# Kernel tuning notes

Measured on AMD Instinct MI355X. Metric: run time of the kernel, lower is better.

The kernel has to match this reference:

```python
import jax, jax.numpy as jnp
import numpy as np

B, L, D = 4, 4096, 1024
K = D // 4

def setup_inputs() -> dict:
    key = jax.random.key(0)
    ks = jax.random.split(key, 16)
    def w(k, sh):
        return jax.random.normal(k, sh, dtype=jnp.float32) * 0.02
    return {
        'x': jax.random.normal(ks[0], (B, L, D), dtype=jnp.float32),
        'Wk1': w(ks[1], (D, D)), 'bk1': jnp.zeros((D,), jnp.float32),
        'Wk2': w(ks[2], (D, K * 4)), 'bk2': jnp.zeros((K * 4,), jnp.float32),
        'Wq1': w(ks[3], (D, D)), 'bq1': jnp.zeros((D,), jnp.float32),
        'Wq2': w(ks[4], (D, K * 4)), 'bq2': jnp.zeros((K * 4,), jnp.float32),
        'Wv': w(ks[5], (D, D)), 'bv': jnp.zeros((D,), jnp.float32),
        'gamma': jnp.ones((D,), jnp.float32), 'beta': jnp.zeros((D,), jnp.float32),
        'Wo': w(ks[6], (D, D)), 'bo': jnp.zeros((D,), jnp.float32),
    }

def _normalize(q, eps=1e-12):
    n = jnp.sqrt(jnp.sum(q * q, axis=-1, keepdims=True))
    return q / jnp.maximum(n, eps)

def _quat_conj(q):
    return q * jnp.asarray([1., -1., -1., -1.], dtype=q.dtype)

def _quat_mul(q1, q2):
    w1, x1, y1, z1 = q1[..., 0], q1[..., 1], q1[..., 2], q1[..., 3]
    w2, x2, y2, z2 = q2[..., 0], q2[..., 1], q2[..., 2], q2[..., 3]
    w = w1 * w2 - x1 * x2 - y1 * y2 - z1 * z2
    x = w1 * x2 + x1 * w2 + y1 * z2 - z1 * y2
    y = w1 * y2 - x1 * z2 + y1 * w2 + z1 * x2
    z = w1 * z2 + x1 * y2 - y1 * x2 + z1 * w2
    return jnp.stack([w, x, y, z], axis=-1)

def _quat_rotate(q, v):
    return _quat_mul(_quat_mul(q, v), _quat_conj(q))

def _mlp(x, W1, b1, W2, b2):
    h = jax.nn.gelu(x @ W1 + b1, approximate=False)
    return h @ W2 + b2

def _layernorm(x, g, b, eps=1e-5):
    mu = jnp.mean(x, axis=-1, keepdims=True)
    var = jnp.var(x, axis=-1, keepdims=True)
    return (x - mu) * jax.lax.rsqrt(var + eps) * g + b

def reference(x, Wk1, bk1, Wk2, bk2, Wq1, bq1, Wq2, bq2, Wv, bv, gamma, beta, Wo, bo):
    b, l, d = x.shape
    k = d // 4
    key_q = _normalize(_mlp(x, Wk1, bk1, Wk2, bk2).reshape(b, l, k, 4))
    query_q = _normalize(_mlp(x, Wq1, bq1, Wq2, bq2).reshape(b, l, k, 4))
    value = (x @ Wv + bv).reshape(b, l, k, 4)
    rotated = _quat_rotate(key_q, value)            # [B,L,K,4]
    memory = jnp.cumsum(rotated, axis=1)            # prefix-sum memory
    retrieved = _quat_rotate(_quat_conj(query_q), memory).reshape(b, l, d)
    norm = jnp.sqrt(jnp.arange(1, l + 1, dtype=x.dtype)).reshape(1, l, 1)
    out = _layernorm(retrieved / norm, gamma, beta) @ Wo + bo
    return x + out
```

## Files before the change

kernel.cpp:

```cpp
#include <hip/hip_runtime.h>
#include <cstddef>
#include <cstdint>

static constexpr int Bb  = 4;
static constexpr int Ll  = 4096;
static constexpr int Mm  = 16384;
static constexpr int KK  = 1024;
static constexpr int NT2 = 16;

typedef __attribute__((ext_vector_type(8))) short short8;
typedef __attribute__((ext_vector_type(4))) float f32x4;

#define AS1C(p) ((const __attribute__((address_space(1))) void*)(p))
#define AS3(p)  ((__attribute__((address_space(3))) void*)(p))

__device__ __forceinline__ float b2f(unsigned short u) {
    union { unsigned int i; float f; } c; c.i = ((unsigned int)u) << 16; return c.f;
}
__device__ __forceinline__ unsigned short f2b(float f) {
    union { float f; unsigned int i; } c; c.f = f;
    unsigned int r = c.i + 0x7fffu + ((c.i >> 16) & 1u);
    return (unsigned short)(r >> 16);
}
__device__ __forceinline__ float4 qmul(const float4 a, const float4 b) {
    float4 r;
    r.x = a.x * b.x - a.y * b.y - a.z * b.z - a.w * b.w;
    r.y = a.x * b.y + a.y * b.x + a.z * b.w - a.w * b.z;
    r.z = a.x * b.z - a.y * b.w + a.z * b.x + a.w * b.y;
    r.w = a.x * b.w + a.y * b.z - a.z * b.y + a.w * b.x;
    return r;
}
__device__ __forceinline__ float4 qconj(const float4 a) {
    return make_float4(a.x, -a.y, -a.z, -a.w);
}
__device__ __forceinline__ float4 qnorm(const float4 a) {
    float n = sqrtf(a.x * a.x + a.y * a.y + a.z * a.z + a.w * a.w);
    float inv = 1.0f / fmaxf(n, 1e-12f);
    return make_float4(a.x * inv, a.y * inv, a.z * inv, a.w * inv);
}
__device__ __forceinline__ float gelu_fast(float v) {
    const float a = fabsf(v) * 0.70710678118654752f;
    const float t = 1.0f / (1.0f + 0.3275911f * a);
    const float p = t * (0.254829592f + t * (-0.284496736f + t * (1.421413741f
                   + t * (-1.453152027f + t * 1.061405429f))));
    const float e = __expf(-a * a);
    const float erfa = 1.0f - p * e;
    return 0.5f * v * (1.0f + copysignf(erfa, v));
}

__global__ __launch_bounds__(256)
void conv_k(const float* __restrict__ src, unsigned short* __restrict__ dst, int n4)
{
    const int i = blockIdx.x * 256 + threadIdx.x;
    if (i >= n4) return;
    const float4 v = reinterpret_cast<const float4*>(src)[i];
    ushort4 o;
    o.x = f2b(v.x); o.y = f2b(v.y); o.z = f2b(v.z); o.w = f2b(v.w);
    reinterpret_cast<ushort4*>(dst)[i] = o;
}

__global__ __launch_bounds__(256)
void wtrans_k(const float* __restrict__ src, unsigned short* __restrict__ dst)
{
    __shared__ float t[32][33];
    const int tx = threadIdx.x, ty = threadIdx.y;
    const int n0 = blockIdx.x * 32, k0 = blockIdx.y * 32;
    #pragma unroll
    for (int j = ty; j < 32; j += 8)
        t[j][tx] = src[(size_t)(k0 + j) * 1024 + n0 + tx];
    __syncthreads();
    #pragma unroll
    for (int j = ty; j < 32; j += 8)
        dst[(size_t)(n0 + j) * 1024 + k0 + tx] = f2b(t[tx][j]);
}

__global__ __launch_bounds__(256)
void bcat_k(const float* __restrict__ bk1, const float* __restrict__ bq1,
            const float* __restrict__ bv,  const float* __restrict__ bk2,
            const float* __restrict__ bq2, float* __restrict__ b1,
            float* __restrict__ b2)
{
    const int i = blockIdx.x * 256 + threadIdx.x;
    if (i < 3072) b1[i] = (i < 1024) ? bk1[i] : (i < 2048 ? bq1[i - 1024] : bv[i - 2048]);
    if (i < 2048) b2[i] = (i < 1024) ? bk2[i] : bq2[i - 1024];
}

template<int MODE>
__global__ __launch_bounds__(512, 2)
void gemm256_k(const unsigned short* __restrict__ A, int astride,
               const unsigned short* __restrict__ BT,
               const float* __restrict__ bias,
               const float* __restrict__ resid,
               unsigned short* __restrict__ outH,
               float* __restrict__ outF,
               int Nn)
{
    extern __shared__ char smem[];
    const int tid  = threadIdx.x;
    const int lane = tid & 63;
    const int w    = tid >> 6;
    const int wr   = w >> 2;
    const int wc   = w & 3;

    const int nwg = gridDim.x;
    const int cpx = nwg >> 3;
    const int bid = blockIdx.x;
    const int swz = (bid & 7) * cpx + (bid >> 3);
    const int nTN = Nn >> 8;
    const int m0  = (swz / nTN) << 8;
    const int n0  = (swz % nTN) << 8;
    const int aoff = (MODE == 1 && n0 >= 1024) ? 1024 : 0;

    const unsigned short* pA[2];
    const unsigned short* pB[2];
    #pragma unroll
    for (int c2 = 0; c2 < 2; ++c2) {
        const int s = c2 * 512 + tid;
        const int line = s >> 3;
        const int v = (s & 7) ^ (line & 7);
        const int r = 2 * line + (v >> 2);
        const int kcs = v & 3;
        pA[c2] = A + (size_t)(m0 + r) * astride + aoff + kcs * 8;
        pB[c2] = BT + (size_t)(n0 + r) * KK + kcs * 8;
    }

    auto STAGE_UNIT = [&](int cdst, int matB, int khs, int t1) {
        const int ks = t1 * 64 + khs * 32;
        #pragma unroll
        for (int c2 = 0; c2 < 2; ++c2) {
            __builtin_amdgcn_global_load_lds(
                AS1C((matB ? pB[c2] : pA[c2]) + ks),
                AS3(smem + cdst * 65536 + matB * 32768 + khs * 16384 + c2 * 8192 + w * 1024),
                16, 0, 0);
        }
    };

    const int kc = lane >> 4;
    const int rl = lane & 15;
    int offA[8], offB[4];
    #pragma unroll
    for (int mi = 0; mi < 8; ++mi) {
        const int r = wr * 128 + mi * 16 + rl;
        offA[mi] = (r >> 1) * 128 + (((((r & 1) << 2) | kc) ^ ((r >> 1) & 7)) << 4);
    }
    #pragma unroll
    for (int ni = 0; ni < 4; ++ni) {
        const int r = wc * 64 + ni * 16 + rl;
        offB[ni] = 32768 + (r >> 1) * 128 + (((((r & 1) << 2) | kc) ^ ((r >> 1) & 7)) << 4);
    }

    f32x4 acc[8][4] = {};
    short8 af[8];

    auto PHASE = [&](int c, int kh, int nh, int su, int t1, int vm) {
        const int base = c * 65536 + kh * 16384;
        if (nh == 0) {
            #pragma unroll
            for (int mi = 0; mi < 8; ++mi)
                af[mi] = *(const short8*)(smem + base + offA[mi]);
        }
        const short8 b0 = *(const short8*)(smem + base + offB[2 * nh + 0]);
        const short8 b1 = *(const short8*)(smem + base + offB[2 * nh + 1]);
        if (su >= 0) STAGE_UNIT(c ^ 1, su & 1, su >> 1, t1);
        __builtin_amdgcn_s_setprio(1);
        #pragma unroll
        for (int mi = 0; mi < 8; ++mi) {
            acc[mi][2 * nh + 0] = __builtin_amdgcn_mfma_f32_16x16x32_bf16(af[mi], b0, acc[mi][2 * nh + 0], 0, 0, 0);
            acc[mi][2 * nh + 1] = __builtin_amdgcn_mfma_f32_16x16x32_bf16(af[mi], b1, acc[mi][2 * nh + 1], 0, 0, 0);
        }
        __builtin_amdgcn_s_setprio(0);
        if (vm == 4)      asm volatile("s_waitcnt vmcnt(4)" ::: "memory");
        else if (vm == 0) asm volatile("s_waitcnt vmcnt(0)" ::: "memory");
        if (vm >= -1) __builtin_amdgcn_s_barrier();
    };

    STAGE_UNIT(0, 0, 0, 0);
    STAGE_UNIT(0, 1, 0, 0);
    STAGE_UNIT(0, 0, 1, 0);
    STAGE_UNIT(0, 1, 1, 0);
    asm volatile("s_waitcnt vmcnt(0)" ::: "memory");
    __builtin_amdgcn_s_barrier();

    for (int t = 0; t < NT2 - 1; ++t) {
        const int c = t & 1;
        PHASE(c, 0, 0, 0, t + 1, 4);
        PHASE(c, 0, 1, 1, t + 1, 4);
        PHASE(c, 1, 0, 2, t + 1, 4);
        PHASE(c, 1, 1, 3, t + 1, 4);
    }
    PHASE(1, 0, 0, -1, 0, -1);
    PHASE(1, 0, 1, -1, 0, 0);
    PHASE(1, 1, 0, -1, 0, -2);
    PHASE(1, 1, 1, -1, 0, -2);
    __syncthreads();

    const int colb = n0 + wc * 64 + rl;
    const int rowb = m0 + wr * 128 + kc * 4;
    float bv[4];
    #pragma unroll
    for (int ni = 0; ni < 4; ++ni) bv[ni] = bias[colb + ni * 16];

    const bool bf16out = (MODE == 1) || (MODE == 0 && n0 < 2048);
    if (bf16out) {
        unsigned short* eb = (unsigned short*)smem;
        const int er = tid >> 2, eq = tid & 3;
        #pragma unroll
        for (int pass = 0; pass < 2; ++pass) {
            if (wr == pass) {
                #pragma unroll
                for (int ni = 0; ni < 4; ++ni) {
                    const int col = wc * 64 + ni * 16 + rl;
                    #pragma unroll
                    for (int mi = 0; mi < 8; ++mi)
                        #pragma unroll
                        for (int rr = 0; rr < 4; ++rr) {
                            float v = acc[mi][ni][rr] + bv[ni];
                            if (MODE == 0) v = gelu_fast(v);
                            eb[(mi * 16 + kc * 4 + rr) * 264 + col] = f2b(v);
                        }
                }
            }
            __syncthreads();
            const size_t grow = (size_t)(m0 + pass * 128 + er) * 2048 + n0 + eq * 64;
            #pragma unroll
            for (int j = 0; j < 8; ++j) {
                *(uint4*)(outH + grow + j * 8) =
                    *(const uint4*)(eb + er * 264 + eq * 64 + j * 8);
            }
            __syncthreads();
        }
    } else {
        #pragma unroll
        for (int ni = 0; ni < 4; ++ni) {
            const int col = colb + ni * 16;
            #pragma unroll
            for (int mi = 0; mi < 8; ++mi) {
                #pragma unroll
                for (int rr = 0; rr < 4; ++rr) {
                    float v = acc[mi][ni][rr] + bv[ni];
                    const int row = rowb + mi * 16 + rr;
                    if (MODE == 0) {
                        outF[(size_t)row * 1024 + (col - 2048)] = v;
                    } else {
                        const size_t ix = (size_t)row * 1024 + col;
                        outF[ix] = v + resid[ix];
                    }
                }
            }
        }
    }
}

__global__ __launch_bounds__(256)
void rotfuse_k(const unsigned short* __restrict__ qb2, float* __restrict__ val,
               float* __restrict__ part)
{
    const int idx = blockIdx.x * 256 + threadIdx.x;
    const int kq  = idx & 255;
    const int ch  = (idx >> 8) & 63;
    const int b   = idx >> 14;
    const int row0 = b * Ll + ch * 64;
    float4 s = make_float4(0.f, 0.f, 0.f, 0.f);
    for (int i = 0; i < 64; ++i) {
        const int row = row0 + i;
        const ushort4 qu = *reinterpret_cast<const ushort4*>(qb2 + (size_t)row * 2048 + kq * 4);
        const float4 q = qnorm(make_float4(b2f(qu.x), b2f(qu.y), b2f(qu.z), b2f(qu.w)));
        float4* vp = reinterpret_cast<float4*>(val + (size_t)row * 1024 + kq * 4);
        const float4 r = qmul(qmul(q, *vp), qconj(q));
        *vp = r;
        s.x += r.x; s.y += r.y; s.z += r.z; s.w += r.w;
    }
    *reinterpret_cast<float4*>(part + (size_t)idx * 4) = s;
}

__global__ __launch_bounds__(256)
void scan2_k(float* __restrict__ part)
{
    const int idx = blockIdx.x * 256 + threadIdx.x;
    const int kq = idx & 255, b = idx >> 8;
    float4 run = make_float4(0.f, 0.f, 0.f, 0.f);
    for (int c = 0; c < 64; ++c) {
        float4* p = reinterpret_cast<float4*>(part + (((size_t)(b * 64 + c)) * 256 + kq) * 4);
        const float4 t = *p;
        *p = run;
        run.x += t.x; run.y += t.y; run.z += t.z; run.w += t.w;
    }
}

__global__ __launch_bounds__(256)
void scan3_k(float* __restrict__ val, const float* __restrict__ part)
{
    const int idx = blockIdx.x * 256 + threadIdx.x;
    const int kq  = idx & 255;
    const int ch  = (idx >> 8) & 63;
    const int b   = idx >> 14;
    const int row0 = b * Ll + ch * 64;
    float4 run = *reinterpret_cast<const float4*>(part + (size_t)idx * 4);
    for (int i = 0; i < 64; ++i) {
        float4* vp = reinterpret_cast<float4*>(val + (size_t)(row0 + i) * 1024 + kq * 4);
        const float4 v = *vp;
        run.x += v.x; run.y += v.y; run.z += v.z; run.w += v.w;
        *vp = run;
    }
}

__global__ __launch_bounds__(256)
void retrieve_ln_k(const float* __restrict__ mem, const unsigned short* __restrict__ qb2,
                   const float* __restrict__ gamma, const float* __restrict__ beta,
                   unsigned short* __restrict__ out)
{
    const int row = blockIdx.x;
    const int l   = row & (Ll - 1);
    const int t   = threadIdx.x;
    const size_t base = (size_t)row * 1024 + t * 4;

    const ushort4 qu = *reinterpret_cast<const ushort4*>(qb2 + (size_t)row * 2048 + 1024 + t * 4);
    const float4 q = qnorm(make_float4(b2f(qu.x), b2f(qu.y), b2f(qu.z), b2f(qu.w)));
    const float4 m4 = *reinterpret_cast<const float4*>(mem + base);
    float4 r = qmul(qmul(qconj(q), m4), q);

    const float inv = 1.0f / sqrtf((float)(l + 1));
    r.x *= inv; r.y *= inv; r.z *= inv; r.w *= inv;

    float s  = r.x + r.y + r.z + r.w;
    float ss = r.x * r.x + r.y * r.y + r.z * r.z + r.w * r.w;
    #pragma unroll
    for (int off = 32; off > 0; off >>= 1) {
        s  += __shfl_xor(s, off);
        ss += __shfl_xor(ss, off);
    }
    __shared__ float red[2][4];
    const int wid = t >> 6, lane = t & 63;
    if (lane == 0) { red[0][wid] = s; red[1][wid] = ss; }
    __syncthreads();
    const float sum = red[0][0] + red[0][1] + red[0][2] + red[0][3];
    const float ssq = red[1][0] + red[1][1] + red[1][2] + red[1][3];
    const float mu  = sum * (1.0f / 1024.0f);
    const float var = ssq * (1.0f / 1024.0f) - mu * mu;
    const float sc  = rsqrtf(var + 1e-5f);

    const float4 g4 = *reinterpret_cast<const float4*>(gamma + t * 4);
    const float4 b4 = *reinterpret_cast<const float4*>(beta  + t * 4);
    ushort4 o;
    o.x = f2b((r.x - mu) * sc * g4.x + b4.x);
    o.y = f2b((r.y - mu) * sc * g4.y + b4.y);
    o.z = f2b((r.z - mu) * sc * g4.z + b4.z);
    o.w = f2b((r.w - mu) * sc * g4.w + b4.w);
    *reinterpret_cast<ushort4*>(out + base) = o;
}

extern "C" void kernel_launch(void* const* d_in, const int* in_sizes, int n_in,
                              void* d_out, int out_size, void* d_ws, size_t ws_size,
                              hipStream_t stream)
{
    const float* x     = (const float*)d_in[0];
    const float* Wk1   = (const float*)d_in[1];
    const float* bk1   = (const float*)d_in[2];
    const float* Wk2   = (const float*)d_in[3];
    const float* bk2   = (const float*)d_in[4];
    const float* Wq1   = (const float*)d_in[5];
    const float* bq1   = (const float*)d_in[6];
    const float* Wq2   = (const float*)d_in[7];
    const float* bq2   = (const float*)d_in[8];
    const float* Wv    = (const float*)d_in[9];
    const float* bv    = (const float*)d_in[10];
    const float* gamma = (const float*)d_in[11];
    const float* beta  = (const float*)d_in[12];
    const float* Wo    = (const float*)d_in[13];
    const float* bo    = (const float*)d_in[14];
    float* out = (float*)d_out;

    const size_t TD = (size_t)Mm * 1024;
    const size_t DD = (size_t)1024 * 1024;

    unsigned short* qb2   = (unsigned short*)d_ws;
    unsigned short* xb    = qb2;
    unsigned short* wcat1 = qb2 + TD;
    unsigned short* h     = qb2 + 2 * TD;
    float*          bufB  = (float*)(h + 2 * TD);
    unsigned short* wcat2 = (unsigned short*)(bufB + TD);
    unsigned short* woT   = wcat2 + 2 * DD;
    float*          bcat1 = (float*)(woT + DD);
    float*          bcat2 = bcat1 + 3072;
    float*          part  = bcat2 + 2048;

    const dim3 blk(256);
    const dim3 tblk(32, 8);
    const dim3 tgrid(32, 32);

    (void)hipFuncSetAttribute((const void*)gemm256_k<0>, hipFuncAttributeMaxDynamicSharedMemorySize, 131072);
    (void)hipFuncSetAttribute((const void*)gemm256_k<1>, hipFuncAttributeMaxDynamicSharedMemorySize, 131072);
    (void)hipFuncSetAttribute((const void*)gemm256_k<2>, hipFuncAttributeMaxDynamicSharedMemorySize, 131072);

    conv_k<<<(int)(TD / 4 / 256), blk, 0, stream>>>(x, xb, (int)(TD / 4));
    wtrans_k<<<tgrid, tblk, 0, stream>>>(Wk1, wcat1);
    wtrans_k<<<tgrid, tblk, 0, stream>>>(Wq1, wcat1 + DD);
    wtrans_k<<<tgrid, tblk, 0, stream>>>(Wv,  wcat1 + 2 * DD);
    wtrans_k<<<tgrid, tblk, 0, stream>>>(Wk2, wcat2);
    wtrans_k<<<tgrid, tblk, 0, stream>>>(Wq2, wcat2 + DD);
    wtrans_k<<<tgrid, tblk, 0, stream>>>(Wo,  woT);
    bcat_k<<<12, blk, 0, stream>>>(bk1, bq1, bv, bk2, bq2, bcat1, bcat2);

    gemm256_k<0><<<64 * 12, 512, 131072, stream>>>(xb, 1024, wcat1, bcat1, nullptr, h, bufB, 3072);
    gemm256_k<1><<<64 * 8, 512, 131072, stream>>>(h, 2048, wcat2, bcat2, nullptr, qb2, nullptr, 2048);

    rotfuse_k<<<256, blk, 0, stream>>>(qb2, bufB, part);
    scan2_k<<<4, blk, 0, stream>>>(part);
    scan3_k<<<256, blk, 0, stream>>>(bufB, part);

    retrieve_ln_k<<<Mm, blk, 0, stream>>>(bufB, qb2, gamma, beta, h);

    gemm256_k<2><<<64 * 4, 512, 131072, stream>>>(h, 1024, woT, bo, x, nullptr, out, 1024);
}
```

Before: 480.6 us.

## Restructure GEMM pipeline, store value in bf16, fuse scan with retrieve-layernorm

```diff
diff --git a/kernel.cpp b/kernel.cpp
--- a/kernel.cpp
+++ b/kernel.cpp
@@ -6,7 +6,8 @@
 static constexpr int Ll  = 4096;
 static constexpr int Mm  = 16384;
 static constexpr int KK  = 1024;
-static constexpr int NT2 = 16;
+static constexpr int NCH = 128;
+static constexpr int CHL = 32;
 
 typedef __attribute__((ext_vector_type(8))) short short8;
 typedef __attribute__((ext_vector_type(4))) float f32x4;
@@ -21,6 +22,12 @@
     union { float f; unsigned int i; } c; c.f = f;
     unsigned int r = c.i + 0x7fffu + ((c.i >> 16) & 1u);
     return (unsigned short)(r >> 16);
+}
+__device__ __forceinline__ float4 bq2f(ushort4 u) {
+    return make_float4(b2f(u.x), b2f(u.y), b2f(u.z), b2f(u.w));
+}
+__device__ __forceinline__ ushort4 f2bq(float4 v) {
+    ushort4 o; o.x = f2b(v.x); o.y = f2b(v.y); o.z = f2b(v.z); o.w = f2b(v.w); return o;
 }
 __device__ __forceinline__ float4 qmul(const float4 a, const float4 b) {
     float4 r;
@@ -54,9 +61,7 @@
     const int i = blockIdx.x * 256 + threadIdx.x;
     if (i >= n4) return;
     const float4 v = reinterpret_cast<const float4*>(src)[i];
-    ushort4 o;
-    o.x = f2b(v.x); o.y = f2b(v.y); o.z = f2b(v.z); o.w = f2b(v.w);
-    reinterpret_cast<ushort4*>(dst)[i] = o;
+    reinterpret_cast<ushort4*>(dst)[i] = f2bq(v);
 }
 
 __global__ __launch_bounds__(256)
@@ -92,6 +97,7 @@
                const float* __restrict__ bias,
                const float* __restrict__ resid,
                unsigned short* __restrict__ outH,
+               unsigned short* __restrict__ outV,
                float* __restrict__ outF,
                int Nn)
 {
@@ -124,13 +130,12 @@
         pB[c2] = BT + (size_t)(n0 + r) * KK + kcs * 8;
     }
 
-    auto STAGE_UNIT = [&](int cdst, int matB, int khs, int t1) {
-        const int ks = t1 * 64 + khs * 32;
+    auto STAGE = [&](int matB, int slot, int kh, int koff) {
         #pragma unroll
         for (int c2 = 0; c2 < 2; ++c2) {
             __builtin_amdgcn_global_load_lds(
-                AS1C((matB ? pB[c2] : pA[c2]) + ks),
-                AS3(smem + cdst * 65536 + matB * 32768 + khs * 16384 + c2 * 8192 + w * 1024),
+                AS1C((matB ? pB[c2] : pA[c2]) + koff),
+                AS3(smem + matB * 65536 + slot * 32768 + kh * 16384 + c2 * 8192 + w * 1024),
                 16, 0, 0);
         }
     };
@@ -146,62 +151,89 @@
     #pragma unroll
     for (int ni = 0; ni < 4; ++ni) {
         const int r = wc * 64 + ni * 16 + rl;
-        offB[ni] = 32768 + (r >> 1) * 128 + (((((r & 1) << 2) | kc) ^ ((r >> 1) & 7)) << 4);
+        offB[ni] = (r >> 1) * 128 + (((((r & 1) << 2) | kc) ^ ((r >> 1) & 7)) << 4);
     }
 
     f32x4 acc[8][4] = {};
     short8 af[8];
 
-    auto PHASE = [&](int c, int kh, int nh, int su, int t1, int vm) {
-        const int base = c * 65536 + kh * 16384;
-        if (nh == 0) {
+    auto PHASE = [&](int slot, int kh, int nih, int smat, int sslot, int skh,
+                     int skoff, int vm) {
+        const int ub = slot * 32768 + kh * 16384;
+        if (nih == 0) {
             #pragma unroll
             for (int mi = 0; mi < 8; ++mi)
-                af[mi] = *(const short8*)(smem + base + offA[mi]);
-        }
-        const short8 b0 = *(const short8*)(smem + base + offB[2 * nh + 0]);
-        const short8 b1 = *(const short8*)(smem + base + offB[2 * nh + 1]);
-        if (su >= 0) STAGE_UNIT(c ^ 1, su & 1, su >> 1, t1);
+                af[mi] = *(const short8*)(smem + ub + offA[mi]);
+        }
+        const short8 b0 = *(const short8*)(smem + 65536 + ub + offB[2 * nih + 0]);
+        const short8 b1 = *(const short8*)(smem + 65536 + ub + offB[2 * nih + 1]);
+        if (smat >= 0) STAGE(smat, sslot, skh, skoff);
+        __builtin_amdgcn_s_barrier();
         __builtin_amdgcn_s_setprio(1);
         #pragma unroll
         for (int mi = 0; mi < 8; ++mi) {
-            acc[mi][2 * nh + 0] = __builtin_amdgcn_mfma_f32_16x16x32_bf16(af[mi], b0, acc[mi][2 * nh + 0], 0, 0, 0);
-            acc[mi][2 * nh + 1] = __builtin_amdgcn_mfma_f32_16x16x32_bf16(af[mi], b1, acc[mi][2 * nh + 1], 0, 0, 0);
+            acc[mi][2 * nih + 0] = __builtin_amdgcn_mfma_f32_16x16x32_bf16(af[mi], b0, acc[mi][2 * nih + 0], 0, 0, 0);
+            acc[mi][2 * nih + 1] = __builtin_amdgcn_mfma_f32_16x16x32_bf16(af[mi], b1, acc[mi][2 * nih + 1], 0, 0, 0);
         }
         __builtin_amdgcn_s_setprio(0);
         if (vm == 4)      asm volatile("s_waitcnt vmcnt(4)" ::: "memory");
         else if (vm == 0) asm volatile("s_waitcnt vmcnt(0)" ::: "memory");
-        if (vm >= -1) __builtin_amdgcn_s_barrier();
+        __builtin_amdgcn_s_barrier();
     };
 
-    STAGE_UNIT(0, 0, 0, 0);
-    STAGE_UNIT(0, 1, 0, 0);
-    STAGE_UNIT(0, 0, 1, 0);
-    STAGE_UNIT(0, 1, 1, 0);
-    asm volatile("s_waitcnt vmcnt(0)" ::: "memory");
+    STAGE(0, 0, 0, 0);  STAGE(1, 0, 0, 0);
+    STAGE(0, 0, 1, 32); STAGE(1, 0, 1, 32);
+    STAGE(0, 1, 0, 64); STAGE(1, 1, 0, 64);
+    asm volatile("s_waitcnt vmcnt(4)" ::: "memory");
     __builtin_amdgcn_s_barrier();
 
-    for (int t = 0; t < NT2 - 1; ++t) {
-        const int c = t & 1;
-        PHASE(c, 0, 0, 0, t + 1, 4);
-        PHASE(c, 0, 1, 1, t + 1, 4);
-        PHASE(c, 1, 0, 2, t + 1, 4);
-        PHASE(c, 1, 1, 3, t + 1, 4);
-    }
-    PHASE(1, 0, 0, -1, 0, -1);
-    PHASE(1, 0, 1, -1, 0, 0);
-    PHASE(1, 1, 0, -1, 0, -2);
-    PHASE(1, 1, 1, -1, 0, -2);
+    for (int i = 0; i < 7; ++i) {
+        const int kb = i * 128;
+        PHASE(0, 0, 0,  0, 1, 1, kb + 96,  -1);
+        PHASE(0, 0, 1,  1, 1, 1, kb + 96,  -1);
+        PHASE(0, 1, 0,  0, 0, 0, kb + 128, -1);
+        PHASE(0, 1, 1,  1, 0, 0, kb + 128,  4);
+        PHASE(1, 0, 0,  0, 0, 1, kb + 160, -1);
+        PHASE(1, 0, 1,  1, 0, 1, kb + 160, -1);
+        PHASE(1, 1, 0,  0, 1, 0, kb + 192, -1);
+        PHASE(1, 1, 1,  1, 1, 0, kb + 192,  4);
+    }
+    PHASE(0, 0, 0,  0, 1, 1, 992, -1);
+    PHASE(0, 0, 1,  1, 1, 1, 992, -1);
+    PHASE(0, 1, 0, -1, 0, 0, 0,   -1);
+    PHASE(0, 1, 1, -1, 0, 0, 0,    0);
+    PHASE(1, 0, 0, -1, 0, 0, 0,   -1);
+    PHASE(1, 0, 1, -1, 0, 0, 0,   -1);
+    PHASE(1, 1, 0, -1, 0, 0, 0,   -1);
+    PHASE(1, 1, 1, -1, 0, 0, 0,   -1);
     __syncthreads();
 
     const int colb = n0 + wc * 64 + rl;
-    const int rowb = m0 + wr * 128 + kc * 4;
     float bv[4];
     #pragma unroll
     for (int ni = 0; ni < 4; ++ni) bv[ni] = bias[colb + ni * 16];
 
-    const bool bf16out = (MODE == 1) || (MODE == 0 && n0 < 2048);
-    if (bf16out) {
+    if (MODE == 2) {
+        const int rowb = m0 + wr * 128 + kc * 4;
+        #pragma unroll
+        for (int ni = 0; ni < 4; ++ni) {
+            const int col = colb + ni * 16;
+            #pragma unroll
+            for (int mi = 0; mi < 8; ++mi) {
+                #pragma unroll
+                for (int rr = 0; rr < 4; ++rr) {
+                    const int row = rowb + mi * 16 + rr;
+                    const size_t ix = (size_t)row * 1024 + col;
+                    outF[ix] = acc[mi][ni][rr] + bv[ni] + resid[ix];
+                }
+            }
+        }
+    } else {
+        const bool dogelu = (MODE == 0) && (n0 < 2048);
+        unsigned short* dst;
+        int stride, col0;
+        if (MODE == 0 && n0 >= 2048) { dst = outV; stride = 1024; col0 = n0 - 2048; }
+        else                         { dst = outH; stride = 2048; col0 = n0; }
         unsigned short* eb = (unsigned short*)smem;
         const int er = tid >> 2, eq = tid & 3;
         #pragma unroll
@@ -211,63 +243,42 @@
                 for (int ni = 0; ni < 4; ++ni) {
                     const int col = wc * 64 + ni * 16 + rl;
                     #pragma unroll
-                    for (int mi = 0; mi < 8; ++mi)
+                    for (int mi = 0; mi < 8; ++mi) {
                         #pragma unroll
                         for (int rr = 0; rr < 4; ++rr) {
                             float v = acc[mi][ni][rr] + bv[ni];
-                            if (MODE == 0) v = gelu_fast(v);
+                            if (dogelu) v = gelu_fast(v);
                             eb[(mi * 16 + kc * 4 + rr) * 264 + col] = f2b(v);
                         }
+                    }
                 }
             }
             __syncthreads();
-            const size_t grow = (size_t)(m0 + pass * 128 + er) * 2048 + n0 + eq * 64;
+            const size_t grow = (size_t)(m0 + pass * 128 + er) * stride + col0 + eq * 64;
             #pragma unroll
-            for (int j = 0; j < 8; ++j) {
-                *(uint4*)(outH + grow + j * 8) =
-                    *(const uint4*)(eb + er * 264 + eq * 64 + j * 8);
-            }
+            for (int j = 0; j < 8; ++j)
+                *(uint4*)(dst + grow + j * 8) = *(const uint4*)(eb + er * 264 + eq * 64 + j * 8);
             __syncthreads();
         }
-    } else {
-        #pragma unroll
-        for (int ni = 0; ni < 4; ++ni) {
-            const int col = colb + ni * 16;
-            #pragma unroll
-            for (int mi = 0; mi < 8; ++mi) {
-                #pragma unroll
-                for (int rr = 0; rr < 4; ++rr) {
-                    float v = acc[mi][ni][rr] + bv[ni];
-                    const int row = rowb + mi * 16 + rr;
-                    if (MODE == 0) {
-                        outF[(size_t)row * 1024 + (col - 2048)] = v;
-                    } else {
-                        const size_t ix = (size_t)row * 1024 + col;
-                        outF[ix] = v + resid[ix];
-                    }
-                }
-            }
-        }
-    }
-}
-
-__global__ __launch_bounds__(256)
-void rotfuse_k(const unsigned short* __restrict__ qb2, float* __restrict__ val,
+    }
+}
+
+__global__ __launch_bounds__(256)
+void rotfuse_k(const unsigned short* __restrict__ qb2, unsigned short* __restrict__ valb,
                float* __restrict__ part)
 {
     const int idx = blockIdx.x * 256 + threadIdx.x;
     const int kq  = idx & 255;
-    const int ch  = (idx >> 8) & 63;
-    const int b   = idx >> 14;
-    const int row0 = b * Ll + ch * 64;
+    const int ch  = (idx >> 8) & 127;
+    const int b   = idx >> 15;
+    const int row0 = b * Ll + ch * CHL;
     float4 s = make_float4(0.f, 0.f, 0.f, 0.f);
-    for (int i = 0; i < 64; ++i) {
+    for (int i = 0; i < CHL; ++i) {
         const int row = row0 + i;
-        const ushort4 qu = *reinterpret_cast<const ushort4*>(qb2 + (size_t)row * 2048 + kq * 4);
-        const float4 q = qnorm(make_float4(b2f(qu.x), b2f(qu.y), b2f(qu.z), b2f(qu.w)));
-        float4* vp = reinterpret_cast<float4*>(val + (size_t)row * 1024 + kq * 4);
-        const float4 r = qmul(qmul(q, *vp), qconj(q));
-        *vp = r;
+        const float4 q = qnorm(bq2f(*reinterpret_cast<const ushort4*>(qb2 + (size_t)row * 2048 + kq * 4)));
+        ushort4* vp = reinterpret_cast<ushort4*>(valb + (size_t)row * 1024 + kq * 4);
+        const float4 r = qmul(qmul(q, bq2f(*vp)), qconj(q));
+        *vp = f2bq(r);
         s.x += r.x; s.y += r.y; s.z += r.z; s.w += r.w;
     }
     *reinterpret_cast<float4*>(part + (size_t)idx * 4) = s;
@@ -279,8 +290,8 @@
     const int idx = blockIdx.x * 256 + threadIdx.x;
     const int kq = idx & 255, b = idx >> 8;
     float4 run = make_float4(0.f, 0.f, 0.f, 0.f);
-    for (int c = 0; c < 64; ++c) {
-        float4* p = reinterpret_cast<float4*>(part + (((size_t)(b * 64 + c)) * 256 + kq) * 4);
+    for (int c = 0; c < NCH; ++c) {
+        float4* p = reinterpret_cast<float4*>(part + (((size_t)(b * NCH + c)) * 256 + kq) * 4);
         const float4 t = *p;
         *p = run;
         run.x += t.x; run.y += t.y; run.z += t.z; run.w += t.w;
@@ -288,65 +299,54 @@
 }
 
 __global__ __launch_bounds__(256)
-void scan3_k(float* __restrict__ val, const float* __restrict__ part)
-{
-    const int idx = blockIdx.x * 256 + threadIdx.x;
-    const int kq  = idx & 255;
-    const int ch  = (idx >> 8) & 63;
-    const int b   = idx >> 14;
-    const int row0 = b * Ll + ch * 64;
-    float4 run = *reinterpret_cast<const float4*>(part + (size_t)idx * 4);
-    for (int i = 0; i < 64; ++i) {
-        float4* vp = reinterpret_cast<float4*>(val + (size_t)(row0 + i) * 1024 + kq * 4);
-        const float4 v = *vp;
+void scan3ln_k(const unsigned short* __restrict__ rotb, const float* __restrict__ part,
+               const unsigned short* __restrict__ qb2,
+               const float* __restrict__ gamma, const float* __restrict__ beta,
+               unsigned short* __restrict__ ln)
+{
+    const int kq = threadIdx.x;
+    const int ch = blockIdx.x & (NCH - 1);
+    const int b  = blockIdx.x >> 7;
+    const int row0 = b * Ll + ch * CHL;
+    float4 run = *reinterpret_cast<const float4*>(part + (((size_t)(b * NCH + ch)) * 256 + kq) * 4);
+
+    __shared__ float red[2][2][4];
+    const int wid = kq >> 6, lane = kq & 63;
+    const float4 g4 = *reinterpret_cast<const float4*>(gamma + kq * 4);
+    const float4 b4 = *reinterpret_cast<const float4*>(beta  + kq * 4);
+
+    for (int i = 0; i < CHL; ++i) {
+        const int row = row0 + i;
+        const float4 v = bq2f(*reinterpret_cast<const ushort4*>(rotb + (size_t)row * 1024 + kq * 4));
         run.x += v.x; run.y += v.y; run.z += v.z; run.w += v.w;
-        *vp = run;
-    }
-}
-
-__global__ __launch_bounds__(256)
-void retrieve_ln_k(const float* __restrict__ mem, const unsigned short* __restrict__ qb2,
-                   const float* __restrict__ gamma, const float* __restrict__ beta,
-                   unsigned short* __restrict__ out)
-{
-    const int row = blockIdx.x;
-    const int l   = row & (Ll - 1);
-    const int t   = threadIdx.x;
-    const size_t base = (size_t)row * 1024 + t * 4;
-
-    const ushort4 qu = *reinterpret_cast<const ushort4*>(qb2 + (size_t)row * 2048 + 1024 + t * 4);
-    const float4 q = qnorm(make_float4(b2f(qu.x), b2f(qu.y), b2f(qu.z), b2f(qu.w)));
-    const float4 m4 = *reinterpret_cast<const float4*>(mem + base);
-    float4 r = qmul(qmul(qconj(q), m4), q);
-
-    const float inv = 1.0f / sqrtf((float)(l + 1));
-    r.x *= inv; r.y *= inv; r.z *= inv; r.w *= inv;
-
-    float s  = r.x + r.y + r.z + r.w;
-    float ss = r.x * r.x + r.y * r.y + r.z * r.z + r.w * r.w;
-    #pragma unroll
-    for (int off = 32; off > 0; off >>= 1) {
-        s  += __shfl_xor(s, off);
-        ss += __shfl_xor(ss, off);
-    }
-    __shared__ float red[2][4];
-    const int wid = t >> 6, lane = t & 63;
-    if (lane == 0) { red[0][wid] = s; red[1][wid] = ss; }
-    __syncthreads();
-    const float sum = red[0][0] + red[0][1] + red[0][2] + red[0][3];
-    const float ssq = red[1][0] + red[1][1] + red[1][2] + red[1][3];
-    const float mu  = sum * (1.0f / 1024.0f);
-    const float var = ssq * (1.0f / 1024.0f) - mu * mu;
-    const float sc  = rsqrtf(var + 1e-5f);
-
-    const float4 g4 = *reinterpret_cast<const float4*>(gamma + t * 4);
-    const float4 b4 = *reinterpret_cast<const float4*>(beta  + t * 4);
-    ushort4 o;
-    o.x = f2b((r.x - mu) * sc * g4.x + b4.x);
-    o.y = f2b((r.y - mu) * sc * g4.y + b4.y);
-    o.z = f2b((r.z - mu) * sc * g4.z + b4.z);
-    o.w = f2b((r.w - mu) * sc * g4.w + b4.w);
-    *reinterpret_cast<ushort4*>(out + base) = o;
+
+        const float4 q = qnorm(bq2f(*reinterpret_cast<const ushort4*>(qb2 + (size_t)row * 2048 + 1024 + kq * 4)));
+        float4 r = qmul(qmul(qconj(q), run), q);
+        const float inv = rsqrtf((float)(ch * CHL + i + 1));
+        r.x *= inv; r.y *= inv; r.z *= inv; r.w *= inv;
+
+        float s  = r.x + r.y + r.z + r.w;
+        float ss = r.x * r.x + r.y * r.y + r.z * r.z + r.w * r.w;
+        #pragma unroll
+        for (int off = 32; off > 0; off >>= 1) {
+            s  += __shfl_xor(s, off);
+            ss += __shfl_xor(ss, off);
+        }
+        if (lane == 0) { red[i & 1][0][wid] = s; red[i & 1][1][wid] = ss; }
+        __syncthreads();
+        const float sum = red[i & 1][0][0] + red[i & 1][0][1] + red[i & 1][0][2] + red[i & 1][0][3];
+        const float ssq = red[i & 1][1][0] + red[i & 1][1][1] + red[i & 1][1][2] + red[i & 1][1][3];
+        const float mu  = sum * (1.0f / 1024.0f);
+        const float var = ssq * (1.0f / 1024.0f) - mu * mu;
+        const float sc  = rsqrtf(var + 1e-5f);
+
+        float4 o;
+        o.x = (r.x - mu) * sc * g4.x + b4.x;
+        o.y = (r.y - mu) * sc * g4.y + b4.y;
+        o.z = (r.z - mu) * sc * g4.z + b4.z;
+        o.w = (r.w - mu) * sc * g4.w + b4.w;
+        *reinterpret_cast<ushort4*>(ln + (size_t)row * 1024 + kq * 4) = f2bq(o);
+    }
 }
 
 extern "C" void kernel_launch(void* const* d_in, const int* in_sizes, int n_in,
@@ -377,8 +377,8 @@
     unsigned short* xb    = qb2;
     unsigned short* wcat1 = qb2 + TD;
     unsigned short* h     = qb2 + 2 * TD;
-    float*          bufB  = (float*)(h + 2 * TD);
-    unsigned short* wcat2 = (unsigned short*)(bufB + TD);
+    unsigned short* valb  = h + 2 * TD;
+    unsigned short* wcat2 = valb + TD;
     unsigned short* woT   = wcat2 + 2 * DD;
     float*          bcat1 = (float*)(woT + DD);
     float*          bcat2 = bcat1 + 3072;
@@ -401,14 +401,12 @@
     wtrans_k<<<tgrid, tblk, 0, stream>>>(Wo,  woT);
     bcat_k<<<12, blk, 0, stream>>>(bk1, bq1, bv, bk2, bq2, bcat1, bcat2);
 
-    gemm256_k<0><<<64 * 12, 512, 131072, stream>>>(xb, 1024, wcat1, bcat1, nullptr, h, bufB, 3072);
-    gemm256_k<1><<<64 * 8, 512, 131072, stream>>>(h, 2048, wcat2, bcat2, nullptr, qb2, nullptr, 2048);
-
-    rotfuse_k<<<256, blk, 0, stream>>>(qb2, bufB, part);
+    gemm256_k<0><<<64 * 12, 512, 131072, stream>>>(xb, 1024, wcat1, bcat1, nullptr, h, valb, nullptr, 3072);
+    gemm256_k<1><<<64 * 8, 512, 131072, stream>>>(h, 2048, wcat2, bcat2, nullptr, qb2, nullptr, nullptr, 2048);
+
+    rotfuse_k<<<(Bb * NCH * 256) / 256, blk, 0, stream>>>(qb2, valb, part);
     scan2_k<<<4, blk, 0, stream>>>(part);
-    scan3_k<<<256, blk, 0, stream>>>(bufB, part);
-
-    retrieve_ln_k<<<Mm, blk, 0, stream>>>(bufB, qb2, gamma, beta, h);
-
-    gemm256_k<2><<<64 * 4, 512, 131072, stream>>>(h, 1024, woT, bo, x, nullptr, out, 1024);
-}
+    scan3ln_k<<<Bb * NCH, blk, 0, stream>>>(valb, part, qb2, gamma, beta, h);
+
+    gemm256_k<2><<<64 * 4, 512, 131072, stream>>>(h, 1024, woT, bo, x, nullptr, nullptr, out, 1024);
+}
```

Measured after the change: 457.3 us. 1.05x faster.
